# Performance work log

Hardware: AMD Instinct MI355X
Metric: run time of the kernel (lower is better)

The kernel has to match this reference:

```python
import jax, jax.numpy as jnp
import numpy as np

V, E, H, T, S = 100000, 300, 512, 5, 4096
START, STOP = 3, 4  # tag_to_ix['<START>'], tag_to_ix['<STOP>']
NEG = -10000.0


def setup_inputs() -> dict:
    key = jax.random.key(0)
    ks = jax.random.split(key, 14)
    sentence = jax.random.randint(ks[0], (S,), 0, V)
    tags = jax.random.randint(ks[1], (S,), 0, 3)  # real tags only (O/B/I)
    sc = 0.05
    embedding = jax.random.normal(ks[2], (V, E), jnp.float32) * sc
    # torch LSTM params, gate order [i, f, g, o]; forward and backward directions
    w_ih_f = jax.random.normal(ks[3], (4 * H, E), jnp.float32) * sc
    w_hh_f = jax.random.normal(ks[4], (4 * H, H), jnp.float32) * sc
    b_ih_f = jax.random.normal(ks[5], (4 * H,), jnp.float32) * sc
    b_hh_f = jax.random.normal(ks[6], (4 * H,), jnp.float32) * sc
    w_ih_b = jax.random.normal(ks[7], (4 * H, E), jnp.float32) * sc
    w_hh_b = jax.random.normal(ks[8], (4 * H, H), jnp.float32) * sc
    b_ih_b = jax.random.normal(ks[9], (4 * H,), jnp.float32) * sc
    b_hh_b = jax.random.normal(ks[10], (4 * H,), jnp.float32) * sc
    w_tag = jax.random.normal(ks[11], (T, 2 * H), jnp.float32) * sc
    b_tag = jax.random.normal(ks[12], (T,), jnp.float32) * sc
    transitions = jax.random.normal(ks[13], (T, T), jnp.float32)
    transitions = transitions.at[START, :].set(NEG).at[:, STOP].set(NEG)
    return dict(sentence=sentence, tags=tags, embedding=embedding,
                w_ih_f=w_ih_f, w_hh_f=w_hh_f, b_ih_f=b_ih_f, b_hh_f=b_hh_f,
                w_ih_b=w_ih_b, w_hh_b=w_hh_b, b_ih_b=b_ih_b, b_hh_b=b_hh_b,
                w_tag=w_tag, b_tag=b_tag, transitions=transitions)


def _lstm(x, w_ih, w_hh, b_ih, b_hh, reverse):
    # x: [S, E]. Precompute input projection once (big GEMM outside scan).
    h = w_hh.shape[1]
    xp = x @ w_ih.T + (b_ih + b_hh)  # [S, 4H]
    def step(carry, xt):
        hp, cp = carry
        g = xt + hp @ w_hh.T
        i, f, gg, o = jnp.split(g, 4)
        c = jax.nn.sigmoid(f) * cp + jax.nn.sigmoid(i) * jnp.tanh(gg)
        hn = jax.nn.sigmoid(o) * jnp.tanh(c)
        return (hn, c), hn
    init = (jnp.zeros((h,), x.dtype), jnp.zeros((h,), x.dtype))
    _, hs = jax.lax.scan(step, init, xp, reverse=reverse)
    return hs  # [S, H]


def reference(sentence, tags, embedding,
              w_ih_f, w_hh_f, b_ih_f, b_hh_f,
              w_ih_b, w_hh_b, b_ih_b, b_hh_b,
              w_tag, b_tag, transitions):
    # _get_lstm_features: embedding -> BiLSTM -> linear
    emb = embedding[sentence]                              # [S, E]
    hf = _lstm(emb, w_ih_f, w_hh_f, b_ih_f, b_hh_f, False)  # [S, H]
    hb = _lstm(emb, w_ih_b, w_hh_b, b_ih_b, b_hh_b, True)   # [S, H]
    feats = jnp.concatenate([hf, hb], axis=-1) @ w_tag.T + b_tag  # [S, T]

    # _forward_alg: CRF log-partition via logsumexp scan
    alpha0 = jnp.full((T,), NEG, feats.dtype).at[START].set(0.0)
    def crf_step(alpha, feat):
        # alpha_new[j] = logsumexp_i(alpha[i] + trans[j, i]) + feat[j]
        a = jax.nn.logsumexp(alpha[None, :] + transitions, axis=1) + feat
        return a, None
    alpha, _ = jax.lax.scan(crf_step, alpha0, feats)
    forward_score = jax.nn.logsumexp(alpha + transitions[STOP])

    # _score_sentence: gold path score
    tags_ext = jnp.concatenate([jnp.array([START], tags.dtype), tags])
    gold = (jnp.sum(transitions[tags_ext[1:], tags_ext[:-1]])
            + jnp.sum(feats[jnp.arange(S), tags])
            + transitions[STOP, tags[-1]])
    return forward_score - gold  # neg_log_likelihood (scalar)
```

## Files before the change

kernel.cpp:

```cpp
#include <hip/hip_runtime.h>
#include <hip/hip_bf16.h>

#define S_LEN 4096
#define EDIM  300
#define HDIM  512
#define G4    2048
#define NTAG  5
#define NEGV  -10000.0f
#define START_TAG 3
#define STOP_TAG  4
#define L2E 1.4426950408889634f
#define LN2 0.6931471805599453f
#define POIS_U 0x7F7F7F7Fu

typedef __attribute__((ext_vector_type(4))) float f32x4;

static constexpr size_t OFF_XP    = 0;
static constexpr size_t XP_BYTES  = (size_t)2 * S_LEN * G4 * 2;
static constexpr size_t OFF_HBS   = OFF_XP + XP_BYTES;
static constexpr size_t HBS_BYTES = (size_t)2 * S_LEN * HDIM * 4;
static constexpr size_t OFF_FEATS = OFF_HBS + HBS_BYTES;
static constexpr size_t OFF_MPART = OFF_FEATS + (size_t)S_LEN * NTAG * 4;
static constexpr size_t OFF_GOLD  = OFF_MPART + (size_t)64 * 25 * 4;
static constexpr size_t WS_NEEDED = OFF_GOLD + 256;

static __device__ __forceinline__ float fexp_(float x){ return __builtin_amdgcn_exp2f(x * L2E); }
static __device__ __forceinline__ float fsig_(float x){ return __builtin_amdgcn_rcpf(1.0f + fexp_(-x)); }
static __device__ __forceinline__ float ftanh_(float x){ return 1.0f - 2.0f*__builtin_amdgcn_rcpf(fexp_(2.0f*x) + 1.0f); }

static __device__ __forceinline__ float lse5(float t0,float t1,float t2,float t3,float t4){
  float m = fmaxf(fmaxf(fmaxf(t0,t1),fmaxf(t2,t3)),t4);
  float s = __builtin_amdgcn_exp2f((t0-m)*L2E) + __builtin_amdgcn_exp2f((t1-m)*L2E)
          + __builtin_amdgcn_exp2f((t2-m)*L2E) + __builtin_amdgcn_exp2f((t3-m)*L2E)
          + __builtin_amdgcn_exp2f((t4-m)*L2E);
  return m + __builtin_amdgcn_logf(s)*LN2;
}

static __device__ __forceinline__ float lse_mm(float cur, float bv, int i, int j){
  const float a0=__shfl(cur, i*5+0), a1=__shfl(cur, i*5+1), a2=__shfl(cur, i*5+2),
              a3=__shfl(cur, i*5+3), a4=__shfl(cur, i*5+4);
  const float c0=__shfl(bv, 0+j),  c1=__shfl(bv, 5+j),  c2=__shfl(bv, 10+j),
              c3=__shfl(bv, 15+j), c4=__shfl(bv, 20+j);
  return lse5(a0+c0, a1+c1, a2+c2, a3+c3, a4+c4);
}

__global__ __launch_bounds__(256) void fill_poison(float* __restrict__ p, int n4){
  const int idx = blockIdx.x*blockDim.x + threadIdx.x;
  const int stride = gridDim.x*blockDim.x;
  f32x4 pv;
  pv.x = __uint_as_float(POIS_U); pv.y = __uint_as_float(POIS_U);
  pv.z = __uint_as_float(POIS_U); pv.w = __uint_as_float(POIS_U);
  for (int i = idx; i < n4; i += stride) {
    float* dst = p + (size_t)i*4;
    asm volatile("global_store_dwordx4 %0, %1, off sc0 sc1" :: "v"(dst), "v"(pv) : "memory");
  }
}

__global__ __launch_bounds__(256) void xp_gemm(
    const int* __restrict__ sentence, const float* __restrict__ emb,
    const float* __restrict__ w_ih_f, const float* __restrict__ b_ih_f, const float* __restrict__ b_hh_f,
    const float* __restrict__ w_ih_b, const float* __restrict__ b_ih_b, const float* __restrict__ b_hh_b,
    __hip_bfloat16* __restrict__ xp)
{
  __shared__ float At[32][132];
  __shared__ float Bt[32][132];
  __shared__ int sent_s[128];

  const int dir = blockIdx.y;
  const int tm = blockIdx.x & 31;
  const int tn = blockIdx.x >> 5;
  const float* __restrict__ wih = dir ? w_ih_b : w_ih_f;
  const float* __restrict__ bi  = dir ? b_ih_b : b_ih_f;
  const float* __restrict__ bh  = dir ? b_hh_b : b_hh_f;

  const int tid = threadIdx.x;
  if (tid < 128) sent_s[tid] = sentence[tm*128 + tid];

  const int ty = tid >> 4, tx = tid & 15;
  const int li = tid >> 1, lh = tid & 1;

  float acc[8][8];
#pragma unroll
  for (int i = 0; i < 8; ++i){
#pragma unroll
    for (int j = 0; j < 8; ++j) acc[i][j] = 0.0f;
  }
  __syncthreads();

  for (int kc0 = 0; kc0 < EDIM; kc0 += 32) {
    const int kw = (EDIM - kc0 < 32) ? (EDIM - kc0) : 32;
    if (kc0 + lh*16 + 16 <= EDIM) {
      const float4* pa = (const float4*)(emb + (size_t)sent_s[li]*EDIM + kc0 + lh*16);
      const float4* pb = (const float4*)(wih + (size_t)(tn*128 + li)*EDIM + kc0 + lh*16);
#pragma unroll
      for (int v = 0; v < 4; ++v) {
        const float4 a = pa[v], b = pb[v];
        const int kk = lh*16 + v*4;
        At[kk+0][li] = a.x; At[kk+1][li] = a.y; At[kk+2][li] = a.z; At[kk+3][li] = a.w;
        Bt[kk+0][li] = b.x; Bt[kk+1][li] = b.y; Bt[kk+2][li] = b.z; Bt[kk+3][li] = b.w;
      }
    } else {
#pragma unroll
      for (int jj = 0; jj < 16; ++jj) {
        const int col = kc0 + lh*16 + jj;
        float av = 0.f, bv = 0.f;
        if (col < EDIM) {
          av = emb[(size_t)sent_s[li]*EDIM + col];
          bv = wih[(size_t)(tn*128 + li)*EDIM + col];
        }
        At[lh*16+jj][li] = av;
        Bt[lh*16+jj][li] = bv;
      }
    }
    __syncthreads();
#pragma unroll 4
    for (int k = 0; k < kw; ++k) {
      const float4 a0 = *(const float4*)&At[k][ty*8];
      const float4 a1 = *(const float4*)&At[k][ty*8+4];
      const float4 b0 = *(const float4*)&Bt[k][tx*8];
      const float4 b1 = *(const float4*)&Bt[k][tx*8+4];
      const float av[8] = {a0.x,a0.y,a0.z,a0.w,a1.x,a1.y,a1.z,a1.w};
      const float bv[8] = {b0.x,b0.y,b0.z,b0.w,b1.x,b1.y,b1.z,b1.w};
#pragma unroll
      for (int i = 0; i < 8; ++i){
#pragma unroll
        for (int j = 0; j < 8; ++j) acc[i][j] = __builtin_fmaf(av[i], bv[j], acc[i][j]);
      }
    }
    __syncthreads();
  }

  const int n0 = tn*128 + tx*8;
  float bias[8];
#pragma unroll
  for (int j = 0; j < 8; ++j) bias[j] = bi[n0+j] + bh[n0+j];

  __hip_bfloat16* __restrict__ xpd = xp + (size_t)dir * S_LEN * G4;
#pragma unroll
  for (int i = 0; i < 8; ++i) {
    const int m = tm*128 + ty*8 + i;
    __hip_bfloat16 __align__(16) tmp[8];
#pragma unroll
    for (int j = 0; j < 8; ++j) tmp[j] = __float2bfloat16(acc[i][j] + bias[j]);
    *(uint4*)(xpd + (size_t)m*G4 + n0) = *(const uint4*)tmp;
  }
}

#define WLOAD0(dst, p) asm volatile("global_load_dwordx4 %0, %1, off"            : "=v"(dst) : "v"(p))
#define WLOAD1(dst, p) asm volatile("global_load_dwordx4 %0, %1, off offset:16"  : "=v"(dst) : "v"(p))
#define ISSUE_W() do { \
    WLOAD0(w0a, wp0); WLOAD1(w0b, wp0); \
    WLOAD0(w1a, wp1); WLOAD1(w1b, wp1); \
    WLOAD0(w2a, wp2); WLOAD1(w2b, wp2); \
    WLOAD0(w3a, wp3); WLOAD1(w3b, wp3); \
  } while (0)

__global__ __launch_bounds__(256, 1) void lstm_pers(
    const float* __restrict__ w_hh_f, const float* __restrict__ w_hh_b,
    const __hip_bfloat16* __restrict__ xp, float* __restrict__ hbs)
{
  const int dir = blockIdx.x >> 7;
  const int wg  = blockIdx.x & 127;
  const int tid = threadIdx.x;
  const int w_  = tid >> 6;
  const int l   = tid & 63;
  const int gu  = wg*4 + w_;

  const float* __restrict__ whh = dir ? w_hh_b : w_hh_f;
  const __hip_bfloat16* __restrict__ xpd = xp + (size_t)dir * S_LEN * G4;
  float* __restrict__ hbs_d = hbs + (size_t)dir * S_LEN * HDIM;

  const float* wp0 = whh + (size_t)(0*HDIM + gu)*HDIM + l*8;
  const float* wp1 = whh + (size_t)(1*HDIM + gu)*HDIM + l*8;
  const float* wp2 = whh + (size_t)(2*HDIM + gu)*HDIM + l*8;
  const float* wp3 = whh + (size_t)(3*HDIM + gu)*HDIM + l*8;

  const __hip_bfloat16* xptr = xpd + (size_t)(dir ? (S_LEN-1) : 0)*G4 + gu;
  const ptrdiff_t xstep = dir ? -(ptrdiff_t)G4 : (ptrdiff_t)G4;
  float xn0 = __bfloat162float(xptr[0*HDIM]);
  float xn1 = __bfloat162float(xptr[1*HDIM]);
  float xn2 = __bfloat162float(xptr[2*HDIM]);
  float xn3 = __bfloat162float(xptr[3*HDIM]);

  float cst = 0.0f;
  f32x4 w0a,w0b,w1a,w1b,w2a,w2b,w3a,w3b;
  ISSUE_W();

  {
    const float iv = fsig_(xn0), fv = fsig_(xn1), zv = ftanh_(xn2), ov = fsig_(xn3);
    cst = fv*0.0f + iv*zv;
    const float hval = ov * ftanh_(cst);
    if (l == 0) {
      float* dp = hbs_d + gu;
      asm volatile("global_store_dword %0, %1, off sc0 sc1" :: "v"(dp), "v"(hval));
    }
    xptr += xstep;
    xn0 = __bfloat162float(xptr[0*HDIM]);
    xn1 = __bfloat162float(xptr[1*HDIM]);
    xn2 = __bfloat162float(xptr[2*HDIM]);
    xn3 = __bfloat162float(xptr[3*HDIM]);
  }

#pragma clang loop unroll(disable)
  for (int s = 1; s < S_LEN; ++s) {
    f32x4 pa, pb;
    const float* sp = hbs_d + (size_t)(s-1)*HDIM + l*8;
    for (int it = 0; it < (1<<18); ++it) {
      asm volatile(
        "global_load_dwordx4 %0, %2, off sc0 sc1\n\t"
        "global_load_dwordx4 %1, %2, off offset:16 sc0 sc1\n\t"
        "s_waitcnt vmcnt(0)"
        : "=&v"(pa), "=&v"(pb) : "v"(sp));
      const int ok = (__float_as_uint(pa.x) != POIS_U) & (__float_as_uint(pa.y) != POIS_U)
                   & (__float_as_uint(pa.z) != POIS_U) & (__float_as_uint(pa.w) != POIS_U)
                   & (__float_as_uint(pb.x) != POIS_U) & (__float_as_uint(pb.y) != POIS_U)
                   & (__float_as_uint(pb.z) != POIS_U) & (__float_as_uint(pb.w) != POIS_U);
      if (__all(ok)) break;
    }

    float a0, a1, a2, a3;
    {
      const float h0=pa.x,h1=pa.y,h2=pa.z,h3=pa.w,h4=pb.x,h5=pb.y,h6=pb.z,h7=pb.w;
      a0 = w0a.x*h0; a0=__builtin_fmaf(w0a.y,h1,a0); a0=__builtin_fmaf(w0a.z,h2,a0); a0=__builtin_fmaf(w0a.w,h3,a0);
      a0=__builtin_fmaf(w0b.x,h4,a0); a0=__builtin_fmaf(w0b.y,h5,a0); a0=__builtin_fmaf(w0b.z,h6,a0); a0=__builtin_fmaf(w0b.w,h7,a0);
      a1 = w1a.x*h0; a1=__builtin_fmaf(w1a.y,h1,a1); a1=__builtin_fmaf(w1a.z,h2,a1); a1=__builtin_fmaf(w1a.w,h3,a1);
      a1=__builtin_fmaf(w1b.x,h4,a1); a1=__builtin_fmaf(w1b.y,h5,a1); a1=__builtin_fmaf(w1b.z,h6,a1); a1=__builtin_fmaf(w1b.w,h7,a1);
      a2 = w2a.x*h0; a2=__builtin_fmaf(w2a.y,h1,a2); a2=__builtin_fmaf(w2a.z,h2,a2); a2=__builtin_fmaf(w2a.w,h3,a2);
      a2=__builtin_fmaf(w2b.x,h4,a2); a2=__builtin_fmaf(w2b.y,h5,a2); a2=__builtin_fmaf(w2b.z,h6,a2); a2=__builtin_fmaf(w2b.w,h7,a2);
      a3 = w3a.x*h0; a3=__builtin_fmaf(w3a.y,h1,a3); a3=__builtin_fmaf(w3a.z,h2,a3); a3=__builtin_fmaf(w3a.w,h3,a3);
      a3=__builtin_fmaf(w3b.x,h4,a3); a3=__builtin_fmaf(w3b.y,h5,a3); a3=__builtin_fmaf(w3b.z,h6,a3); a3=__builtin_fmaf(w3b.w,h7,a3);
    }

    if (s + 1 < S_LEN) ISSUE_W();

    {
      const bool u1 = (l & 1) != 0;
      float m0 = u1 ? a2 : a0, s0_ = u1 ? a0 : a2;
      float m1 = u1 ? a3 : a1, s1_ = u1 ? a1 : a3;
      const float b0 = m0 + __shfl_xor(s0_, 1);
      const float b1 = m1 + __shfl_xor(s1_, 1);
      const bool u2 = (l & 2) != 0;
      float m2 = u2 ? b1 : b0, s2_ = u2 ? b0 : b1;
      float tot = m2 + __shfl_xor(s2_, 2);
      tot += __shfl_xor(tot, 4);
      tot += __shfl_xor(tot, 8);
      tot += __shfl_xor(tot, 16);
      tot += __shfl_xor(tot, 32);

      const float gi = __shfl(tot, 0) + xn0;
      const float gf = __shfl(tot, 2) + xn1;
      const float gg = __shfl(tot, 1) + xn2;
      const float go = __shfl(tot, 3) + xn3;
      const float iv = fsig_(gi), fv = fsig_(gf), zv = ftanh_(gg), ov = fsig_(go);
      cst = fv*cst + iv*zv;
      const float hval = ov * ftanh_(cst);
      if (l == 0) {
        float* dp = hbs_d + (size_t)s*HDIM + gu;
        asm volatile("global_store_dword %0, %1, off sc0 sc1" :: "v"(dp), "v"(hval));
      }
    }

    if (s + 1 < S_LEN) {
      xptr += xstep;
      xn0 = __bfloat162float(xptr[0*HDIM]);
      xn1 = __bfloat162float(xptr[1*HDIM]);
      xn2 = __bfloat162float(xptr[2*HDIM]);
      xn3 = __bfloat162float(xptr[3*HDIM]);
    }
  }
}

__global__ __launch_bounds__(64) void feats_ker(
    const float* __restrict__ hbs, const float* __restrict__ w_tag,
    const float* __restrict__ b_tag, float* __restrict__ feats)
{
  const int row = blockIdx.x;
  const int l = threadIdx.x;
  const float* __restrict__ hf  = hbs + (size_t)row*HDIM;
  const float* __restrict__ hbk = hbs + (size_t)S_LEN*HDIM + (size_t)(S_LEN-1-row)*HDIM;
  float a0=0,a1=0,a2=0,a3=0,a4=0;
#pragma unroll
  for (int i = 0; i < 8; ++i) {
    const int j = l + i*64;
    const float hfv = hf[j];
    const float hbv = hbk[j];
    a0 += hfv*w_tag[0*1024+j] + hbv*w_tag[0*1024+512+j];
    a1 += hfv*w_tag[1*1024+j] + hbv*w_tag[1*1024+512+j];
    a2 += hfv*w_tag[2*1024+j] + hbv*w_tag[2*1024+512+j];
    a3 += hfv*w_tag[3*1024+j] + hbv*w_tag[3*1024+512+j];
    a4 += hfv*w_tag[4*1024+j] + hbv*w_tag[4*1024+512+j];
  }
#pragma unroll
  for (int off = 32; off; off >>= 1) {
    a0 += __shfl_xor(a0, off); a1 += __shfl_xor(a1, off); a2 += __shfl_xor(a2, off);
    a3 += __shfl_xor(a3, off); a4 += __shfl_xor(a4, off);
  }
  if (l == 0) {
    feats[row*NTAG+0] = a0 + b_tag[0];
    feats[row*NTAG+1] = a1 + b_tag[1];
    feats[row*NTAG+2] = a2 + b_tag[2];
    feats[row*NTAG+3] = a3 + b_tag[3];
    feats[row*NTAG+4] = a4 + b_tag[4];
  }
}

__global__ __launch_bounds__(64) void crf_part(
    const float* __restrict__ feats, const float* __restrict__ trans,
    const int* __restrict__ tags, float* __restrict__ Mpart, float* __restrict__ gold_part)
{
  const int blk = blockIdx.x;
  const int l = threadIdx.x;
  const int s0 = blk * 64;
  const bool act = (l < 25);
  const int i = act ? (l/5) : 0;
  const int j = act ? (l%5) : 0;
  const float tT = trans[j*NTAG + i];
  float cur = tT + feats[(size_t)s0*NTAG + j];
  for (int s = s0+1; s < s0+64; ++s) {
    const float bv = tT + feats[(size_t)s*NTAG + j];
    cur = lse_mm(cur, bv, i, j);
  }
  if (act) Mpart[blk*25 + l] = cur;

  const int s = s0 + l;
  const int tg = tags[s];
  const int pv = (s == 0) ? START_TAG : tags[s-1];
  float gv = trans[tg*NTAG + pv] + feats[(size_t)s*NTAG + tg];
#pragma unroll
  for (int off = 32; off; off >>= 1) gv += __shfl_xor(gv, off);
  if (l == 0) gold_part[blk] = gv;
}

__global__ __launch_bounds__(64) void crf_final(
    const float* __restrict__ Mpart, const float* __restrict__ gold_part,
    const float* __restrict__ trans, const int* __restrict__ tags, float* __restrict__ out)
{
  const int l = threadIdx.x;
  const bool act = (l < 25);
  const int i = act ? (l/5) : 0;
  const int j = act ? (l%5) : 0;
  float cur = Mpart[act ? l : 0];
  for (int b = 1; b < 64; ++b) {
    const float bv = Mpart[b*25 + (act ? l : 0)];
    cur = lse_mm(cur, bv, i, j);
  }
  const float t0 = ((0==START_TAG)?0.f:NEGV) + __shfl(cur, 0*5 + j);
  const float t1 = ((1==START_TAG)?0.f:NEGV) + __shfl(cur, 1*5 + j);
  const float t2 = ((2==START_TAG)?0.f:NEGV) + __shfl(cur, 2*5 + j);
  const float t3 = ((3==START_TAG)?0.f:NEGV) + __shfl(cur, 3*5 + j);
  const float t4 = ((4==START_TAG)?0.f:NEGV) + __shfl(cur, 4*5 + j);
  const float aF = lse5(t0,t1,t2,t3,t4);
  const float f0 = __shfl(aF, 0) + trans[STOP_TAG*NTAG + 0];
  const float f1 = __shfl(aF, 1) + trans[STOP_TAG*NTAG + 1];
  const float f2 = __shfl(aF, 2) + trans[STOP_TAG*NTAG + 2];
  const float f3 = __shfl(aF, 3) + trans[STOP_TAG*NTAG + 3];
  const float f4 = __shfl(aF, 4) + trans[STOP_TAG*NTAG + 4];
  const float fwd = lse5(f0,f1,f2,f3,f4);
  float gv = gold_part[l];
#pragma unroll
  for (int off = 32; off; off >>= 1) gv += __shfl_xor(gv, off);
  if (l == 0) out[0] = fwd - (gv + trans[STOP_TAG*NTAG + tags[S_LEN-1]]);
}

extern "C" void kernel_launch(void* const* d_in, const int* in_sizes, int n_in,
                              void* d_out, int out_size, void* d_ws, size_t ws_size,
                              hipStream_t stream) {
  const int*   sentence = (const int*)d_in[0];
  const int*   tags     = (const int*)d_in[1];
  const float* emb      = (const float*)d_in[2];
  const float* w_ih_f   = (const float*)d_in[3];
  const float* w_hh_f   = (const float*)d_in[4];
  const float* b_ih_f   = (const float*)d_in[5];
  const float* b_hh_f   = (const float*)d_in[6];
  const float* w_ih_b   = (const float*)d_in[7];
  const float* w_hh_b   = (const float*)d_in[8];
  const float* b_ih_b   = (const float*)d_in[9];
  const float* b_hh_b   = (const float*)d_in[10];
  const float* w_tag    = (const float*)d_in[11];
  const float* b_tag    = (const float*)d_in[12];
  const float* trans    = (const float*)d_in[13];
  float* out = (float*)d_out;
  char* ws = (char*)d_ws;
  if (ws_size < WS_NEEDED) return;

  __hip_bfloat16* xp   = (__hip_bfloat16*)(ws + OFF_XP);
  float* hbs           = (float*)(ws + OFF_HBS);
  float* feats         = (float*)(ws + OFF_FEATS);
  float* Mpart         = (float*)(ws + OFF_MPART);
  float* gold_part     = (float*)(ws + OFF_GOLD);

  const int n4 = (2 * S_LEN * HDIM) / 4;
  fill_poison<<<dim3(1024), dim3(256), 0, stream>>>(hbs, n4);
  xp_gemm<<<dim3(512, 2, 1), dim3(256), 0, stream>>>(sentence, emb,
      w_ih_f, b_ih_f, b_hh_f, w_ih_b, b_ih_b, b_hh_b, xp);
  lstm_pers<<<dim3(256), dim3(256), 0, stream>>>(w_hh_f, w_hh_b, xp, hbs);
  feats_ker<<<dim3(4096), dim3(64), 0, stream>>>(hbs, w_tag, b_tag, feats);
  crf_part<<<dim3(64), dim3(64), 0, stream>>>(feats, trans, tags, Mpart, gold_part);
  crf_final<<<dim3(1), dim3(64), 0, stream>>>(Mpart, gold_part, trans, tags, out);
}
```

Before: 10.45 ms.

## Publish LSTM hidden state as bf16 with one polling wave per block

The persistent LSTM kernel now stores the hidden state as bf16. The four waves of each workgroup gather their values in LDS so a single 8-byte store publishes them. Only wave 0 polls the global hidden-state row, and it shares what it reads with the other waves through LDS. This cuts the bytes of cross-block polling and the number of polling waves, but adds two __syncthreads per timestep and rounds h to bf16, which lowers accuracy. feats_ker is also changed to read the packed bf16 rows with vector loads.

```diff
diff --git a/kernel.cpp b/kernel.cpp
--- a/kernel.cpp
+++ b/kernel.cpp
@@ -12,8 +12,11 @@
 #define L2E 1.4426950408889634f
 #define LN2 0.6931471805599453f
 #define POIS_U 0x7F7F7F7Fu
+#define HP_ROW 512
 
 typedef __attribute__((ext_vector_type(4))) float f32x4;
+typedef __attribute__((ext_vector_type(4))) unsigned int u32x4;
+typedef __attribute__((ext_vector_type(2))) unsigned int u32x2;
 
 static constexpr size_t OFF_XP    = 0;
 static constexpr size_t XP_BYTES  = (size_t)2 * S_LEN * G4 * 2;
@@ -157,8 +160,11 @@
 
 __global__ __launch_bounds__(256, 1) void lstm_pers(
     const float* __restrict__ w_hh_f, const float* __restrict__ w_hh_b,
-    const __hip_bfloat16* __restrict__ xp, float* __restrict__ hbs)
+    const __hip_bfloat16* __restrict__ xp, unsigned short* __restrict__ hpub)
 {
+  __shared__ u32x4 hbc[64];
+  __shared__ __align__(8) unsigned short hg[8];
+
   const int dir = blockIdx.x >> 7;
   const int wg  = blockIdx.x & 127;
   const int tid = threadIdx.x;
@@ -168,7 +174,7 @@
 
   const float* __restrict__ whh = dir ? w_hh_b : w_hh_f;
   const __hip_bfloat16* __restrict__ xpd = xp + (size_t)dir * S_LEN * G4;
-  float* __restrict__ hbs_d = hbs + (size_t)dir * S_LEN * HDIM;
+  unsigned short* __restrict__ hp = hpub + (size_t)dir * S_LEN * HP_ROW;
 
   const float* wp0 = whh + (size_t)(0*HDIM + gu)*HDIM + l*8;
   const float* wp1 = whh + (size_t)(1*HDIM + gu)*HDIM + l*8;
@@ -188,11 +194,15 @@
 
   {
     const float iv = fsig_(xn0), fv = fsig_(xn1), zv = ftanh_(xn2), ov = fsig_(xn3);
-    cst = fv*0.0f + iv*zv;
+    cst = iv*zv;
     const float hval = ov * ftanh_(cst);
-    if (l == 0) {
-      float* dp = hbs_d + gu;
-      asm volatile("global_store_dword %0, %1, off sc0 sc1" :: "v"(dp), "v"(hval));
+    __hip_bfloat16 hb = __float2bfloat16(hval);
+    if (l == 0) hg[w_] = __builtin_bit_cast(unsigned short, hb);
+    __syncthreads();
+    if (tid == 0) {
+      const u32x2 g = *(const u32x2*)hg;
+      unsigned short* dp = hp + (size_t)0*HP_ROW + wg*4;
+      asm volatile("global_store_dwordx2 %0, %1, off sc0 sc1" :: "v"(dp), "v"(g));
     }
     xptr += xstep;
     xn0 = __bfloat162float(xptr[0*HDIM]);
@@ -203,24 +213,31 @@
 
 #pragma clang loop unroll(disable)
   for (int s = 1; s < S_LEN; ++s) {
-    f32x4 pa, pb;
-    const float* sp = hbs_d + (size_t)(s-1)*HDIM + l*8;
-    for (int it = 0; it < (1<<18); ++it) {
-      asm volatile(
-        "global_load_dwordx4 %0, %2, off sc0 sc1\n\t"
-        "global_load_dwordx4 %1, %2, off offset:16 sc0 sc1\n\t"
-        "s_waitcnt vmcnt(0)"
-        : "=&v"(pa), "=&v"(pb) : "v"(sp));
-      const int ok = (__float_as_uint(pa.x) != POIS_U) & (__float_as_uint(pa.y) != POIS_U)
-                   & (__float_as_uint(pa.z) != POIS_U) & (__float_as_uint(pa.w) != POIS_U)
-                   & (__float_as_uint(pb.x) != POIS_U) & (__float_as_uint(pb.y) != POIS_U)
-                   & (__float_as_uint(pb.z) != POIS_U) & (__float_as_uint(pb.w) != POIS_U);
-      if (__all(ok)) break;
-    }
+    if (w_ == 0) {
+      u32x4 pa;
+      const unsigned short* sp = hp + (size_t)(s-1)*HP_ROW + l*8;
+      for (int it = 0; it < (1<<18); ++it) {
+        asm volatile(
+          "global_load_dwordx4 %0, %1, off sc0 sc1\n\t"
+          "s_waitcnt vmcnt(0)"
+          : "=&v"(pa) : "v"(sp));
+        const int ok = (pa.x != POIS_U) & (pa.y != POIS_U)
+                     & (pa.z != POIS_U) & (pa.w != POIS_U);
+        if (__all(ok)) break;
+      }
+      hbc[l] = pa;
+    }
+    __syncthreads();
+    asm volatile("s_waitcnt vmcnt(0)");
+    __builtin_amdgcn_sched_barrier(0);
 
     float a0, a1, a2, a3;
     {
-      const float h0=pa.x,h1=pa.y,h2=pa.z,h3=pa.w,h4=pb.x,h5=pb.y,h6=pb.z,h7=pb.w;
+      const u32x4 hv = hbc[l];
+      const float h0 = __uint_as_float(hv.x << 16), h1 = __uint_as_float(hv.x & 0xFFFF0000u);
+      const float h2 = __uint_as_float(hv.y << 16), h3 = __uint_as_float(hv.y & 0xFFFF0000u);
+      const float h4 = __uint_as_float(hv.z << 16), h5 = __uint_as_float(hv.z & 0xFFFF0000u);
+      const float h6 = __uint_as_float(hv.w << 16), h7 = __uint_as_float(hv.w & 0xFFFF0000u);
       a0 = w0a.x*h0; a0=__builtin_fmaf(w0a.y,h1,a0); a0=__builtin_fmaf(w0a.z,h2,a0); a0=__builtin_fmaf(w0a.w,h3,a0);
       a0=__builtin_fmaf(w0b.x,h4,a0); a0=__builtin_fmaf(w0b.y,h5,a0); a0=__builtin_fmaf(w0b.z,h6,a0); a0=__builtin_fmaf(w0b.w,h7,a0);
       a1 = w1a.x*h0; a1=__builtin_fmaf(w1a.y,h1,a1); a1=__builtin_fmaf(w1a.z,h2,a1); a1=__builtin_fmaf(w1a.w,h3,a1);
@@ -254,10 +271,8 @@
       const float iv = fsig_(gi), fv = fsig_(gf), zv = ftanh_(gg), ov = fsig_(go);
       cst = fv*cst + iv*zv;
       const float hval = ov * ftanh_(cst);
-      if (l == 0) {
-        float* dp = hbs_d + (size_t)s*HDIM + gu;
-        asm volatile("global_store_dword %0, %1, off sc0 sc1" :: "v"(dp), "v"(hval));
-      }
+      __hip_bfloat16 hb = __float2bfloat16(hval);
+      if (l == 0) hg[w_] = __builtin_bit_cast(unsigned short, hb);
     }
 
     if (s + 1 < S_LEN) {
@@ -267,40 +282,54 @@
       xn2 = __bfloat162float(xptr[2*HDIM]);
       xn3 = __bfloat162float(xptr[3*HDIM]);
     }
+
+    __syncthreads();
+    if (tid == 0) {
+      const u32x2 g = *(const u32x2*)hg;
+      unsigned short* dp = hp + (size_t)s*HP_ROW + wg*4;
+      asm volatile("global_store_dwordx2 %0, %1, off sc0 sc1" :: "v"(dp), "v"(g));
+    }
   }
 }
 
 __global__ __launch_bounds__(64) void feats_ker(
-    const float* __restrict__ hbs, const float* __restrict__ w_tag,
+    const unsigned short* __restrict__ hpub, const float* __restrict__ w_tag,
     const float* __restrict__ b_tag, float* __restrict__ feats)
 {
   const int row = blockIdx.x;
   const int l = threadIdx.x;
-  const float* __restrict__ hf  = hbs + (size_t)row*HDIM;
-  const float* __restrict__ hbk = hbs + (size_t)S_LEN*HDIM + (size_t)(S_LEN-1-row)*HDIM;
-  float a0=0,a1=0,a2=0,a3=0,a4=0;
-#pragma unroll
-  for (int i = 0; i < 8; ++i) {
-    const int j = l + i*64;
-    const float hfv = hf[j];
-    const float hbv = hbk[j];
-    a0 += hfv*w_tag[0*1024+j] + hbv*w_tag[0*1024+512+j];
-    a1 += hfv*w_tag[1*1024+j] + hbv*w_tag[1*1024+512+j];
-    a2 += hfv*w_tag[2*1024+j] + hbv*w_tag[2*1024+512+j];
-    a3 += hfv*w_tag[3*1024+j] + hbv*w_tag[3*1024+512+j];
-    a4 += hfv*w_tag[4*1024+j] + hbv*w_tag[4*1024+512+j];
+  const u32x4 hfv4 = *(const u32x4*)(hpub + (size_t)row*HP_ROW + l*8);
+  const u32x4 hbv4 = *(const u32x4*)(hpub + (size_t)S_LEN*HP_ROW + (size_t)(S_LEN-1-row)*HP_ROW + l*8);
+  float hf[8], hb[8];
+  hf[0]=__uint_as_float(hfv4.x<<16); hf[1]=__uint_as_float(hfv4.x&0xFFFF0000u);
+  hf[2]=__uint_as_float(hfv4.y<<16); hf[3]=__uint_as_float(hfv4.y&0xFFFF0000u);
+  hf[4]=__uint_as_float(hfv4.z<<16); hf[5]=__uint_as_float(hfv4.z&0xFFFF0000u);
+  hf[6]=__uint_as_float(hfv4.w<<16); hf[7]=__uint_as_float(hfv4.w&0xFFFF0000u);
+  hb[0]=__uint_as_float(hbv4.x<<16); hb[1]=__uint_as_float(hbv4.x&0xFFFF0000u);
+  hb[2]=__uint_as_float(hbv4.y<<16); hb[3]=__uint_as_float(hbv4.y&0xFFFF0000u);
+  hb[4]=__uint_as_float(hbv4.z<<16); hb[5]=__uint_as_float(hbv4.z&0xFFFF0000u);
+  hb[6]=__uint_as_float(hbv4.w<<16); hb[7]=__uint_as_float(hbv4.w&0xFFFF0000u);
+
+  float a[5];
+#pragma unroll
+  for (int t = 0; t < 5; ++t) {
+    const float* wt = w_tag + t*1024 + l*8;
+    const float* wb = w_tag + t*1024 + 512 + l*8;
+    float s = 0.f;
+#pragma unroll
+    for (int k = 0; k < 8; ++k) s = __builtin_fmaf(hf[k], wt[k], s);
+#pragma unroll
+    for (int k = 0; k < 8; ++k) s = __builtin_fmaf(hb[k], wb[k], s);
+    a[t] = s;
   }
 #pragma unroll
   for (int off = 32; off; off >>= 1) {
-    a0 += __shfl_xor(a0, off); a1 += __shfl_xor(a1, off); a2 += __shfl_xor(a2, off);
-    a3 += __shfl_xor(a3, off); a4 += __shfl_xor(a4, off);
+    a[0] += __shfl_xor(a[0], off); a[1] += __shfl_xor(a[1], off); a[2] += __shfl_xor(a[2], off);
+    a[3] += __shfl_xor(a[3], off); a[4] += __shfl_xor(a[4], off);
   }
   if (l == 0) {
-    feats[row*NTAG+0] = a0 + b_tag[0];
-    feats[row*NTAG+1] = a1 + b_tag[1];
-    feats[row*NTAG+2] = a2 + b_tag[2];
-    feats[row*NTAG+3] = a3 + b_tag[3];
-    feats[row*NTAG+4] = a4 + b_tag[4];
+#pragma unroll
+    for (int t = 0; t < 5; ++t) feats[row*NTAG+t] = a[t] + b_tag[t];
   }
 }
 
@@ -383,18 +412,18 @@
   char* ws = (char*)d_ws;
   if (ws_size < WS_NEEDED) return;
 
-  __hip_bfloat16* xp   = (__hip_bfloat16*)(ws + OFF_XP);
-  float* hbs           = (float*)(ws + OFF_HBS);
-  float* feats         = (float*)(ws + OFF_FEATS);
-  float* Mpart         = (float*)(ws + OFF_MPART);
-  float* gold_part     = (float*)(ws + OFF_GOLD);
-
-  const int n4 = (2 * S_LEN * HDIM) / 4;
-  fill_poison<<<dim3(1024), dim3(256), 0, stream>>>(hbs, n4);
+  __hip_bfloat16* xp    = (__hip_bfloat16*)(ws + OFF_XP);
+  unsigned short* hpub  = (unsigned short*)(ws + OFF_HBS);
+  float* feats          = (float*)(ws + OFF_FEATS);
+  float* Mpart          = (float*)(ws + OFF_MPART);
+  float* gold_part      = (float*)(ws + OFF_GOLD);
+
+  const int n4 = (2 * S_LEN * HP_ROW * 2) / 16;
+  fill_poison<<<dim3(1024), dim3(256), 0, stream>>>((float*)hpub, n4);
   xp_gemm<<<dim3(512, 2, 1), dim3(256), 0, stream>>>(sentence, emb,
       w_ih_f, b_ih_f, b_hh_f, w_ih_b, b_ih_b, b_hh_b, xp);
-  lstm_pers<<<dim3(256), dim3(256), 0, stream>>>(w_hh_f, w_hh_b, xp, hbs);
-  feats_ker<<<dim3(4096), dim3(64), 0, stream>>>(hbs, w_tag, b_tag, feats);
+  lstm_pers<<<dim3(256), dim3(256), 0, stream>>>(w_hh_f, w_hh_b, xp, hpub);
+  feats_ker<<<dim3(4096), dim3(64), 0, stream>>>(hpub, w_tag, b_tag, feats);
   crf_part<<<dim3(64), dim3(64), 0, stream>>>(feats, trans, tags, Mpart, gold_part);
   crf_final<<<dim3(1), dim3(64), 0, stream>>>(Mpart, gold_part, trans, tags, out);
 }
```

Measured after the change: 13.15 ms. 25.9% more time.
